# Performance work log

Hardware: AMD Instinct MI355X
Metric: run time of the kernel (lower is better)

The kernel has to match this reference:

```python
import jax, jax.numpy as jnp
import numpy as np

N_NODES = 100000
N_EDGES = 1600000
D_IN = 64
D_HID = 64


def setup_inputs() -> dict:
    key = jax.random.key(0)
    k1, k2, k3, k4, k5 = jax.random.split(key, 5)
    features = jax.random.normal(k1, (N_NODES, D_IN), dtype=jnp.float32)
    src = jax.random.randint(k2, (N_EDGES,), 0, N_NODES, dtype=jnp.int64)
    dst = jax.random.randint(k3, (N_EDGES,), 0, N_NODES, dtype=jnp.int64)
    # nn.Linear(in_feats, n_hidden): W is [out, in], b is [out]
    W = jax.random.normal(k4, (D_HID, D_IN), dtype=jnp.float32) * (1.0 / np.sqrt(D_IN))
    b = jax.random.normal(k5, (D_HID,), dtype=jnp.float32) * 0.01
    return {"features": features, "src": src, "dst": dst, "W": W, "b": b}


def reference(features, src, dst, W, b):
    # copy_src + sum: h_agg[v] = sum_{(u->v) in E} features[u]
    msgs = features[src]                                   # [E, D_IN] gather
    h_agg = jax.ops.segment_sum(msgs, dst, num_segments=N_NODES)  # [N, D_IN] scatter-add
    # NodeApplyModule: linear + activation
    h = h_agg @ W.T + b                                    # [N, D_HID]
    return jax.nn.relu(h)
```

## Files before the change

### kernel.cpp

```cpp
#include <hip/hip_runtime.h>
#include <hip/hip_bf16.h>
#include <hip/hip_fp16.h>

constexpr int N_NODES = 100000;
constexpr int N_EDGES = 1600000;
constexpr int D = 64;
constexpr int NPB = 64;
constexpr int NBUK = (N_NODES + NPB - 1) / NPB;
constexpr int CAP = 1536;
constexpr int CAP_E = 2048;
constexpr unsigned SENT = 100000u;
constexpr int PART_BLOCKS = 256;
constexpr int CONV_BLOCKS = 256;
constexpr int PREP_THREADS = 1024;
constexpr int EPB = (N_EDGES + PART_BLOCKS - 1) / PART_BLOCKS;

__global__ __launch_bounds__(PREP_THREADS) void prep_kernel(
    const float* __restrict__ feat, const int* __restrict__ src,
    const int* __restrict__ dst, int* __restrict__ gtot,
    unsigned* __restrict__ packed, uint2* __restrict__ fb) {
    const int tid = threadIdx.x;

    if (blockIdx.x >= PART_BLOCKS) {
        const int cb = blockIdx.x - PART_BLOCKS;
        const int total = N_NODES * D / 4;
        const float4* f4 = reinterpret_cast<const float4*>(feat);
        for (int i = cb * PREP_THREADS + tid; i < total; i += CONV_BLOCKS * PREP_THREADS) {
            const float4 v = f4[i];
            __half2 p0 = __floats2half2_rn(v.x, v.y);
            __half2 p1 = __floats2half2_rn(v.z, v.w);
            fb[i] = make_uint2(*reinterpret_cast<unsigned*>(&p0),
                               *reinterpret_cast<unsigned*>(&p1));
        }
        if (cb == 0 && tid < 16)
            fb[(size_t)SENT * 16 + tid] = make_uint2(0u, 0u);
        return;
    }

    __shared__ int lcnt[NBUK];
    __shared__ int lbase[NBUK];

    const int base = blockIdx.x * EPB + tid;

    int d0 = 0, d1 = 0, d2 = 0, d3 = 0, d4 = 0, d5 = 0, d6 = 0;
    const bool k0 = tid            < EPB, k1 = tid + 1024 < EPB;
    const bool k2 = tid + 2048 < EPB,     k3 = tid + 3072 < EPB;
    const bool k4 = tid + 4096 < EPB,     k5 = tid + 5120 < EPB;
    const bool k6 = tid + 6144 < EPB;
    if (k0) d0 = dst[base];
    if (k1) d1 = dst[base + 1024];
    if (k2) d2 = dst[base + 2048];
    if (k3) d3 = dst[base + 3072];
    if (k4) d4 = dst[base + 4096];
    if (k5) d5 = dst[base + 5120];
    if (k6) d6 = dst[base + 6144];

    for (int i = tid; i < NBUK; i += PREP_THREADS) lcnt[i] = 0;
    __syncthreads();

    if (k0) atomicAdd(&lcnt[d0 >> 6], 1);
    if (k1) atomicAdd(&lcnt[d1 >> 6], 1);
    if (k2) atomicAdd(&lcnt[d2 >> 6], 1);
    if (k3) atomicAdd(&lcnt[d3 >> 6], 1);
    if (k4) atomicAdd(&lcnt[d4 >> 6], 1);
    if (k5) atomicAdd(&lcnt[d5 >> 6], 1);
    if (k6) atomicAdd(&lcnt[d6 >> 6], 1);
    __syncthreads();

    {
        const int start = (int)((blockIdx.x * 997u) % (unsigned)NBUK);
        int i1 = start + tid; if (i1 >= NBUK) i1 -= NBUK;
        const int c1 = lcnt[i1];
        lbase[i1] = c1 ? atomicAdd(&gtot[i1], c1) : 0;
        lcnt[i1] = 0;
        if (tid + PREP_THREADS < NBUK) {
            int i2 = i1 + PREP_THREADS; if (i2 >= NBUK) i2 -= NBUK;
            const int c2 = lcnt[i2];
            lbase[i2] = c2 ? atomicAdd(&gtot[i2], c2) : 0;
            lcnt[i2] = 0;
        }
    }
    __syncthreads();

    #define SCATTER(kk, dd, off)                                              \
        if (kk) {                                                             \
            const int s = src[base + off];                                    \
            const int buk = dd >> 6;                                          \
            const int p = lbase[buk] + atomicAdd(&lcnt[buk], 1);              \
            if (p < CAP)                                                      \
                packed[(size_t)buk * CAP + p] =                               \
                    ((unsigned)(dd & (NPB - 1)) << 17) | (unsigned)s;         \
        }
    SCATTER(k0, d0, 0)
    SCATTER(k1, d1, 1024)
    SCATTER(k2, d2, 2048)
    SCATTER(k3, d3, 3072)
    SCATTER(k4, d4, 4096)
    SCATTER(k5, d5, 5120)
    SCATTER(k6, d6, 6144)
    #undef SCATTER
}

__global__ __launch_bounds__(256, 2) void bucket_kernel(
    const uint2* __restrict__ fb, const int* __restrict__ gtot,
    const unsigned* __restrict__ packed, const float* __restrict__ W,
    const float* __restrict__ bias, float* __restrict__ out) {
    __shared__ unsigned elist[CAP_E];
    __shared__ int cnt[NPB];
    __shared__ int cur[NPB];
    __shared__ int pstart[NPB];
    __shared__ float hrow[4][D];

    const int tid = threadIdx.x;
    const int w = tid >> 6;
    const int j = tid & 63;
    const int g = j >> 4;
    const int l = j & 15;
    const int buk = blockIdx.x;

    float4 wr[16];
    #pragma unroll
    for (int q = 0; q < 16; ++q)
        wr[q] = *reinterpret_cast<const float4*>(W + j * D + (q << 2));
    const float bj = bias[j];

    int m = gtot[buk]; if (m > CAP) m = CAP;
    const unsigned* bp = packed + (size_t)buk * CAP;

    unsigned pk0 = 0, pk1 = 0, pk2 = 0, pk3 = 0, pk4 = 0, pk5 = 0;
    const bool v0 = tid < m,            v1 = tid + 256 < m;
    const bool v2 = tid + 512 < m,      v3 = tid + 768 < m;
    const bool v4 = tid + 1024 < m,     v5 = tid + 1280 < m;
    if (v0) pk0 = bp[tid];
    if (v1) pk1 = bp[tid + 256];
    if (v2) pk2 = bp[tid + 512];
    if (v3) pk3 = bp[tid + 768];
    if (v4) pk4 = bp[tid + 1024];
    if (v5) pk5 = bp[tid + 1280];

    if (tid < NPB) cnt[tid] = 0;
    #pragma unroll
    for (int i = 0; i < CAP_E / 256; ++i) elist[tid + i * 256] = SENT;
    __syncthreads();

    if (v0) atomicAdd(&cnt[pk0 >> 17], 1);
    if (v1) atomicAdd(&cnt[pk1 >> 17], 1);
    if (v2) atomicAdd(&cnt[pk2 >> 17], 1);
    if (v3) atomicAdd(&cnt[pk3 >> 17], 1);
    if (v4) atomicAdd(&cnt[pk4 >> 17], 1);
    if (v5) atomicAdd(&cnt[pk5 >> 17], 1);
    __syncthreads();

    if (tid < 64) {
        const int c = cnt[tid];
        const int pc = (c + 7) & ~7;
        int x = pc;
        #pragma unroll
        for (int o = 1; o < 64; o <<= 1) {
            const int y = __shfl_up(x, o);
            if (tid >= o) x += y;
        }
        pstart[tid] = x - pc;
        cur[tid] = x - pc;
    }
    __syncthreads();

    if (v0) { const int p = atomicAdd(&cur[pk0 >> 17], 1); elist[p] = pk0 & 0x1FFFFu; }
    if (v1) { const int p = atomicAdd(&cur[pk1 >> 17], 1); elist[p] = pk1 & 0x1FFFFu; }
    if (v2) { const int p = atomicAdd(&cur[pk2 >> 17], 1); elist[p] = pk2 & 0x1FFFFu; }
    if (v3) { const int p = atomicAdd(&cur[pk3 >> 17], 1); elist[p] = pk3 & 0x1FFFFu; }
    if (v4) { const int p = atomicAdd(&cur[pk4 >> 17], 1); elist[p] = pk4 & 0x1FFFFu; }
    if (v5) { const int p = atomicAdd(&cur[pk5 >> 17], 1); elist[p] = pk5 & 0x1FFFFu; }
    __syncthreads();

    const int gbase = buk * NPB;
    const int n0 = w << 4;

    const int pf = pstart[n0];
    uint2 q0 = fb[(size_t)elist[pf + g] * 16 + l];
    uint2 q1 = fb[(size_t)elist[pf + 4 + g] * 16 + l];

    const __half2 h2z = __float2half2_rn(0.0f);

    for (int n = n0; n < n0 + 16; ++n) {
        int i = pstart[n];
        const int e1 = i + ((cnt[n] + 7) & ~7);
        const int nextstart = (n + 1 < NPB) ? pstart[n + 1] : 0;

        __half2 a01 = h2z, a23 = h2z;

        while (i < e1) {
            const int i_nxt = (i + 8 < e1) ? (i + 8) : nextstart;
            const int t0 = elist[i_nxt + g];
            const int t1 = elist[i_nxt + 4 + g];
            const uint2 r0 = fb[(size_t)t0 * 16 + l];
            const uint2 r1 = fb[(size_t)t1 * 16 + l];
            a01 = __hadd2(a01, *reinterpret_cast<const __half2*>(&q0.x));
            a23 = __hadd2(a23, *reinterpret_cast<const __half2*>(&q0.y));
            a01 = __hadd2(a01, *reinterpret_cast<const __half2*>(&q1.x));
            a23 = __hadd2(a23, *reinterpret_cast<const __half2*>(&q1.y));
            q0 = r0; q1 = r1;
            i += 8;
        }

        float hx = __low2float(a01), hy = __high2float(a01);
        float hz = __low2float(a23), hw_ = __high2float(a23);

        hx += __shfl_xor(hx, 16); hx += __shfl_xor(hx, 32);
        hy += __shfl_xor(hy, 16); hy += __shfl_xor(hy, 32);
        hz += __shfl_xor(hz, 16); hz += __shfl_xor(hz, 32);
        hw_ += __shfl_xor(hw_, 16); hw_ += __shfl_xor(hw_, 32);

        if (g == 0)
            *reinterpret_cast<float4*>(&hrow[w][l << 2]) =
                make_float4(hx, hy, hz, hw_);

        float acc = bj;
        #pragma unroll
        for (int q = 0; q < 16; ++q) {
            const float4 hv = *reinterpret_cast<const float4*>(&hrow[w][q << 2]);
            acc = fmaf(hv.x, wr[q].x, acc);
            acc = fmaf(hv.y, wr[q].y, acc);
            acc = fmaf(hv.z, wr[q].z, acc);
            acc = fmaf(hv.w, wr[q].w, acc);
        }
        const int gn = gbase + n;
        if (gn < N_NODES) out[(size_t)gn * D + j] = fmaxf(acc, 0.0f);
    }
}

extern "C" void kernel_launch(void* const* d_in, const int* in_sizes, int n_in,
                              void* d_out, int out_size, void* d_ws, size_t ws_size,
                              hipStream_t stream) {
    const float* feat = (const float*)d_in[0];
    const int*   src  = (const int*)d_in[1];
    const int*   dst  = (const int*)d_in[2];
    const float* W    = (const float*)d_in[3];
    const float* b    = (const float*)d_in[4];
    float* out = (float*)d_out;

    int* gtot = (int*)d_ws;
    unsigned* packed = (unsigned*)((char*)d_ws + 8192);
    uint2* fb = (uint2*)((char*)d_ws + 8192 + (size_t)NBUK * CAP * 4);

    hipMemsetAsync(gtot, 0, NBUK * sizeof(int), stream);

    prep_kernel<<<PART_BLOCKS + CONV_BLOCKS, PREP_THREADS, 0, stream>>>(
        feat, src, dst, gtot, packed, fb);

    bucket_kernel<<<NBUK, 256, 0, stream>>>(fb, gtot, packed, W, b, out);
}
```

Before: 95.69 us.

## Apply linear transform before aggregation and split gather into feature slices

Uses linearity to compute Y = X·Wᵀ per node in the prep kernel and store it in fp16, sliced into four 16-column planes. This removes the per-node matmul from the gather stage. The bucket kernel is split into a sort kernel that writes sorted edge lists and offsets back to global memory, and a gather kernel launched with four blocks per bucket, one per column slice, to raise parallelism and shrink each gathered row. The cost is an extra kernel launch and extra global round-trips for the sorted lists. Rounding Y to fp16 before summation also changes where precision is lost.

```diff
diff --git a/kernel.cpp b/kernel.cpp
--- a/kernel.cpp
+++ b/kernel.cpp
@@ -7,33 +7,57 @@
 constexpr int D = 64;
 constexpr int NPB = 64;
 constexpr int NBUK = (N_NODES + NPB - 1) / NPB;
-constexpr int CAP = 1536;
-constexpr int CAP_E = 2048;
+constexpr int CAP2 = 2048;
 constexpr unsigned SENT = 100000u;
+constexpr int SLICE_N = 100001;
 constexpr int PART_BLOCKS = 256;
-constexpr int CONV_BLOCKS = 256;
+constexpr int TRAN_BLOCKS = 256;
 constexpr int PREP_THREADS = 1024;
 constexpr int EPB = (N_EDGES + PART_BLOCKS - 1) / PART_BLOCKS;
 
 __global__ __launch_bounds__(PREP_THREADS) void prep_kernel(
     const float* __restrict__ feat, const int* __restrict__ src,
     const int* __restrict__ dst, int* __restrict__ gtot,
-    unsigned* __restrict__ packed, uint2* __restrict__ fb) {
+    unsigned* __restrict__ seg, uint2* __restrict__ Yt,
+    const float* __restrict__ W) {
     const int tid = threadIdx.x;
 
     if (blockIdx.x >= PART_BLOCKS) {
         const int cb = blockIdx.x - PART_BLOCKS;
-        const int total = N_NODES * D / 4;
-        const float4* f4 = reinterpret_cast<const float4*>(feat);
-        for (int i = cb * PREP_THREADS + tid; i < total; i += CONV_BLOCKS * PREP_THREADS) {
-            const float4 v = f4[i];
-            __half2 p0 = __floats2half2_rn(v.x, v.y);
-            __half2 p1 = __floats2half2_rn(v.z, v.w);
-            fb[i] = make_uint2(*reinterpret_cast<unsigned*>(&p0),
-                               *reinterpret_cast<unsigned*>(&p1));
-        }
-        if (cb == 0 && tid < 16)
-            fb[(size_t)SENT * 16 + tid] = make_uint2(0u, 0u);
+        const int w = tid >> 6;
+        const int j = tid & 63;
+
+        float4 wr[16];
+        #pragma unroll
+        for (int q = 0; q < 16; ++q)
+            wr[q] = *reinterpret_cast<const float4*>(W + j * D + (q << 2));
+
+        if (cb == 0 && tid < 16) {
+            const int s = tid >> 2, part = tid & 3;
+            Yt[((size_t)s * SLICE_N + 100000) * 4 + part] = make_uint2(0u, 0u);
+        }
+
+        for (int node = cb * 16 + w; node < N_NODES; node += TRAN_BLOCKS * 16) {
+            const float* frow = feat + (size_t)node * D;
+            float acc = 0.0f;
+            #pragma unroll
+            for (int q = 0; q < 16; ++q) {
+                const float4 fv = *reinterpret_cast<const float4*>(frow + (q << 2));
+                acc = fmaf(fv.x, wr[q].x, acc);
+                acc = fmaf(fv.y, wr[q].y, acc);
+                acc = fmaf(fv.z, wr[q].z, acc);
+                acc = fmaf(fv.w, wr[q].w, acc);
+            }
+            const float accn = __shfl_down(acc, 1);
+            auto pk = __builtin_amdgcn_cvt_pkrtz(acc, accn);
+            const unsigned u = *reinterpret_cast<const unsigned*>(&pk);
+            const unsigned u2 = __shfl_down(u, 2);
+            if ((j & 3) == 0) {
+                const int chunk = j >> 2;
+                const int s = chunk >> 2, part = chunk & 3;
+                Yt[((size_t)s * SLICE_N + node) * 4 + part] = make_uint2(u, u2);
+            }
+        }
         return;
     }
 
@@ -87,8 +111,8 @@
             const int s = src[base + off];                                    \
             const int buk = dd >> 6;                                          \
             const int p = lbase[buk] + atomicAdd(&lcnt[buk], 1);              \
-            if (p < CAP)                                                      \
-                packed[(size_t)buk * CAP + p] =                               \
+            if (p < CAP2)                                                     \
+                seg[(size_t)buk * CAP2 + p] =                                 \
                     ((unsigned)(dd & (NPB - 1)) << 17) | (unsigned)s;         \
         }
     SCATTER(k0, d0, 0)
@@ -101,131 +125,120 @@
     #undef SCATTER
 }
 
-__global__ __launch_bounds__(256, 2) void bucket_kernel(
-    const uint2* __restrict__ fb, const int* __restrict__ gtot,
-    const unsigned* __restrict__ packed, const float* __restrict__ W,
-    const float* __restrict__ bias, float* __restrict__ out) {
-    __shared__ unsigned elist[CAP_E];
+__global__ __launch_bounds__(256) void sort_kernel(
+    const int* __restrict__ gtot, unsigned* __restrict__ seg,
+    int* __restrict__ pstG) {
+    __shared__ unsigned raw[CAP2];
+    __shared__ unsigned elist[CAP2];
     __shared__ int cnt[NPB];
     __shared__ int cur[NPB];
-    __shared__ int pstart[NPB];
-    __shared__ float hrow[4][D];
+    __shared__ int pst[NPB + 1];
 
     const int tid = threadIdx.x;
-    const int w = tid >> 6;
-    const int j = tid & 63;
-    const int g = j >> 4;
-    const int l = j & 15;
     const int buk = blockIdx.x;
-
-    float4 wr[16];
-    #pragma unroll
-    for (int q = 0; q < 16; ++q)
-        wr[q] = *reinterpret_cast<const float4*>(W + j * D + (q << 2));
-    const float bj = bias[j];
-
-    int m = gtot[buk]; if (m > CAP) m = CAP;
-    const unsigned* bp = packed + (size_t)buk * CAP;
-
-    unsigned pk0 = 0, pk1 = 0, pk2 = 0, pk3 = 0, pk4 = 0, pk5 = 0;
-    const bool v0 = tid < m,            v1 = tid + 256 < m;
-    const bool v2 = tid + 512 < m,      v3 = tid + 768 < m;
-    const bool v4 = tid + 1024 < m,     v5 = tid + 1280 < m;
-    if (v0) pk0 = bp[tid];
-    if (v1) pk1 = bp[tid + 256];
-    if (v2) pk2 = bp[tid + 512];
-    if (v3) pk3 = bp[tid + 768];
-    if (v4) pk4 = bp[tid + 1024];
-    if (v5) pk5 = bp[tid + 1280];
-
+    unsigned* sg = seg + (size_t)buk * CAP2;
+
+    int m = gtot[buk]; if (m > CAP2) m = CAP2;
+
+    for (int i = tid; i < CAP2; i += 256) elist[i] = SENT;
     if (tid < NPB) cnt[tid] = 0;
-    #pragma unroll
-    for (int i = 0; i < CAP_E / 256; ++i) elist[tid + i * 256] = SENT;
-    __syncthreads();
-
-    if (v0) atomicAdd(&cnt[pk0 >> 17], 1);
-    if (v1) atomicAdd(&cnt[pk1 >> 17], 1);
-    if (v2) atomicAdd(&cnt[pk2 >> 17], 1);
-    if (v3) atomicAdd(&cnt[pk3 >> 17], 1);
-    if (v4) atomicAdd(&cnt[pk4 >> 17], 1);
-    if (v5) atomicAdd(&cnt[pk5 >> 17], 1);
+    for (int i = tid; i < m; i += 256) raw[i] = sg[i];
+    __syncthreads();
+
+    for (int i = tid; i < m; i += 256)
+        atomicAdd(&cnt[raw[i] >> 17], 1);
     __syncthreads();
 
     if (tid < 64) {
         const int c = cnt[tid];
-        const int pc = (c + 7) & ~7;
+        const int pc = (c + 15) & ~15;
         int x = pc;
         #pragma unroll
         for (int o = 1; o < 64; o <<= 1) {
             const int y = __shfl_up(x, o);
             if (tid >= o) x += y;
         }
-        pstart[tid] = x - pc;
-        cur[tid] = x - pc;
-    }
-    __syncthreads();
-
-    if (v0) { const int p = atomicAdd(&cur[pk0 >> 17], 1); elist[p] = pk0 & 0x1FFFFu; }
-    if (v1) { const int p = atomicAdd(&cur[pk1 >> 17], 1); elist[p] = pk1 & 0x1FFFFu; }
-    if (v2) { const int p = atomicAdd(&cur[pk2 >> 17], 1); elist[p] = pk2 & 0x1FFFFu; }
-    if (v3) { const int p = atomicAdd(&cur[pk3 >> 17], 1); elist[p] = pk3 & 0x1FFFFu; }
-    if (v4) { const int p = atomicAdd(&cur[pk4 >> 17], 1); elist[p] = pk4 & 0x1FFFFu; }
-    if (v5) { const int p = atomicAdd(&cur[pk5 >> 17], 1); elist[p] = pk5 & 0x1FFFFu; }
-    __syncthreads();
-
+        int e = x - pc; if (e > CAP2 - 16) e = CAP2 - 16;
+        pst[tid] = e;
+        cur[tid] = e;
+        if (tid == 63) {
+            int t = x; if (t > CAP2 - 16) t = CAP2 - 16;
+            pst[64] = t;
+        }
+    }
+    __syncthreads();
+
+    for (int i = tid; i < m; i += 256) {
+        const unsigned pk = raw[i];
+        const int p = atomicAdd(&cur[pk >> 17], 1);
+        if (p < CAP2) elist[p] = pk & 0x1FFFFu;
+    }
+    __syncthreads();
+
+    for (int i = tid; i < CAP2; i += 256) sg[i] = elist[i];
+    if (tid < NPB + 1) pstG[buk * (NPB + 1) + tid] = pst[tid];
+}
+
+__global__ __launch_bounds__(256, 2) void gather_kernel(
+    const uint2* __restrict__ Yt, const unsigned* __restrict__ seg,
+    const int* __restrict__ pstG, const float* __restrict__ bias,
+    float* __restrict__ out) {
+    __shared__ int pst[NPB + 1];
+
+    const int tid = threadIdx.x;
+    const int w = tid >> 6;
+    const int j = tid & 63;
+    const int buk = blockIdx.x >> 2;
+    const int slice = blockIdx.x & 3;
+
+    if (tid < NPB + 1) pst[tid] = pstG[buk * (NPB + 1) + tid];
+    __syncthreads();
+
+    const unsigned* sg = seg + (size_t)buk * CAP2;
+    const uint2* Ys = Yt + (size_t)slice * SLICE_N * 4;
+    const float4 bj4 = *reinterpret_cast<const float4*>(bias + slice * 16 + ((j & 3) << 2));
+
+    const int n0 = w << 4;
+    const int eq = j >> 2;
+    const int ch = j & 3;
+
+    int i = pst[n0];
+    unsigned sv = sg[i + eq];
+    uint2 q = Ys[(size_t)(sv & 0x1FFFFu) * 4 + ch];
+
+    const __half2 h2z = __float2half2_rn(0.0f);
     const int gbase = buk * NPB;
-    const int n0 = w << 4;
-
-    const int pf = pstart[n0];
-    uint2 q0 = fb[(size_t)elist[pf + g] * 16 + l];
-    uint2 q1 = fb[(size_t)elist[pf + 4 + g] * 16 + l];
-
-    const __half2 h2z = __float2half2_rn(0.0f);
 
     for (int n = n0; n < n0 + 16; ++n) {
-        int i = pstart[n];
-        const int e1 = i + ((cnt[n] + 7) & ~7);
-        const int nextstart = (n + 1 < NPB) ? pstart[n + 1] : 0;
-
+        const int e1 = pst[n + 1];
         __half2 a01 = h2z, a23 = h2z;
 
         while (i < e1) {
-            const int i_nxt = (i + 8 < e1) ? (i + 8) : nextstart;
-            const int t0 = elist[i_nxt + g];
-            const int t1 = elist[i_nxt + 4 + g];
-            const uint2 r0 = fb[(size_t)t0 * 16 + l];
-            const uint2 r1 = fb[(size_t)t1 * 16 + l];
-            a01 = __hadd2(a01, *reinterpret_cast<const __half2*>(&q0.x));
-            a23 = __hadd2(a23, *reinterpret_cast<const __half2*>(&q0.y));
-            a01 = __hadd2(a01, *reinterpret_cast<const __half2*>(&q1.x));
-            a23 = __hadd2(a23, *reinterpret_cast<const __half2*>(&q1.y));
-            q0 = r0; q1 = r1;
-            i += 8;
+            const int inx = i + 16;
+            const unsigned snx = sg[inx + eq];
+            const uint2 r = Ys[(size_t)(snx & 0x1FFFFu) * 4 + ch];
+            a01 = __hadd2(a01, *reinterpret_cast<const __half2*>(&q.x));
+            a23 = __hadd2(a23, *reinterpret_cast<const __half2*>(&q.y));
+            q = r; i = inx;
         }
 
         float hx = __low2float(a01), hy = __high2float(a01);
         float hz = __low2float(a23), hw_ = __high2float(a23);
 
-        hx += __shfl_xor(hx, 16); hx += __shfl_xor(hx, 32);
-        hy += __shfl_xor(hy, 16); hy += __shfl_xor(hy, 32);
-        hz += __shfl_xor(hz, 16); hz += __shfl_xor(hz, 32);
-        hw_ += __shfl_xor(hw_, 16); hw_ += __shfl_xor(hw_, 32);
-
-        if (g == 0)
-            *reinterpret_cast<float4*>(&hrow[w][l << 2]) =
-                make_float4(hx, hy, hz, hw_);
-
-        float acc = bj;
-        #pragma unroll
-        for (int q = 0; q < 16; ++q) {
-            const float4 hv = *reinterpret_cast<const float4*>(&hrow[w][q << 2]);
-            acc = fmaf(hv.x, wr[q].x, acc);
-            acc = fmaf(hv.y, wr[q].y, acc);
-            acc = fmaf(hv.z, wr[q].z, acc);
-            acc = fmaf(hv.w, wr[q].w, acc);
-        }
+        hx += __shfl_xor(hx, 4); hx += __shfl_xor(hx, 8); hx += __shfl_xor(hx, 16); hx += __shfl_xor(hx, 32);
+        hy += __shfl_xor(hy, 4); hy += __shfl_xor(hy, 8); hy += __shfl_xor(hy, 16); hy += __shfl_xor(hy, 32);
+        hz += __shfl_xor(hz, 4); hz += __shfl_xor(hz, 8); hz += __shfl_xor(hz, 16); hz += __shfl_xor(hz, 32);
+        hw_ += __shfl_xor(hw_, 4); hw_ += __shfl_xor(hw_, 8); hw_ += __shfl_xor(hw_, 16); hw_ += __shfl_xor(hw_, 32);
+
         const int gn = gbase + n;
-        if (gn < N_NODES) out[(size_t)gn * D + j] = fmaxf(acc, 0.0f);
+        if (j < 4 && gn < N_NODES) {
+            float4 o;
+            o.x = fmaxf(hx + bj4.x, 0.0f);
+            o.y = fmaxf(hy + bj4.y, 0.0f);
+            o.z = fmaxf(hz + bj4.z, 0.0f);
+            o.w = fmaxf(hw_ + bj4.w, 0.0f);
+            *reinterpret_cast<float4*>(out + (size_t)gn * D + slice * 16 + (j << 2)) = o;
+        }
     }
 }
 
@@ -240,13 +253,17 @@
     float* out = (float*)d_out;
 
     int* gtot = (int*)d_ws;
-    unsigned* packed = (unsigned*)((char*)d_ws + 8192);
-    uint2* fb = (uint2*)((char*)d_ws + 8192 + (size_t)NBUK * CAP * 4);
-
-    hipMemsetAsync(gtot, 0, NBUK * sizeof(int), stream);
-
-    prep_kernel<<<PART_BLOCKS + CONV_BLOCKS, PREP_THREADS, 0, stream>>>(
-        feat, src, dst, gtot, packed, fb);
-
-    bucket_kernel<<<NBUK, 256, 0, stream>>>(fb, gtot, packed, W, b, out);
-}
+    unsigned* seg = (unsigned*)((char*)d_ws + 8192);
+    int* pstG = (int*)((char*)d_ws + 8192 + (size_t)NBUK * CAP2 * 4);
+    uint2* Yt = (uint2*)((char*)d_ws + 8192 + (size_t)NBUK * CAP2 * 4
+                         + (size_t)NBUK * (NPB + 1) * 4);
+
+    (void)hipMemsetAsync(gtot, 0, NBUK * sizeof(int), stream);
+
+    prep_kernel<<<PART_BLOCKS + TRAN_BLOCKS, PREP_THREADS, 0, stream>>>(
+        feat, src, dst, gtot, seg, Yt, W);
+
+    sort_kernel<<<NBUK, 256, 0, stream>>>(gtot, seg, pstG);
+
+    gather_kernel<<<NBUK * 4, 256, 0, stream>>>(Yt, seg, pstG, b, out);
+}
```

Measured after the change: 172.7 us. 1.8x slower.
